# Kernel optimization log

Hardware: AMD Instinct MI355X
Metric: run time of the kernel (lower is better)

## Reference

```python
import jax, jax.numpy as jnp
import numpy as np

DIM = 512
NUM_EXPERTS = 16
HIDDEN = 512
OUT_DIM = DIM // 4  # 128


def setup_inputs() -> dict:
    key = jax.random.key(0)
    k_x, k_w1, k_w2 = jax.random.split(key, 3)
    x = jax.random.normal(k_x, (4, 2048, DIM), dtype=jnp.float32)
    # init_(t): uniform(-1/sqrt(last_dim), 1/sqrt(last_dim))
    s1 = 1.0 / np.sqrt(HIDDEN)
    s2 = 1.0 / np.sqrt(OUT_DIM)
    w1 = jax.random.uniform(k_w1, (NUM_EXPERTS, DIM, HIDDEN), dtype=jnp.float32, minval=-s1, maxval=s1)
    w2 = jax.random.uniform(k_w2, (NUM_EXPERTS, HIDDEN, OUT_DIM), dtype=jnp.float32, minval=-s2, maxval=s2)
    return {"x": x, "w1": w1, "w2": w2}


def reference(x, w1, w2):
    # x: [b, n, d]; w1: [e, d, h]; w2: [e, h, d4]
    hidden = jnp.einsum("bnd,edh->benh", x, w1)          # [b, e, n, h]
    hidden = jax.nn.gelu(hidden, approximate=False)       # exact GELU = torch nn.GELU default
    out = jnp.einsum("benh,ehd->bnde", hidden, w2)        # [b, n, d4, e]
    return out
```

## Files before the change

### kernel.cpp

```cpp
#include <hip/hip_runtime.h>
#include <stdint.h>

typedef short bf16x8 __attribute__((ext_vector_type(8)));
typedef float f32x4 __attribute__((ext_vector_type(4)));

__device__ __forceinline__ void async_cp16(const void* g, short* lds) {
  __builtin_amdgcn_global_load_lds(
      (const __attribute__((address_space(1))) void*)g,
      (__attribute__((address_space(3))) void*)lds, 16, 0, 0);
}

__device__ __forceinline__ float gelu_f(float v) {
  float z = 1.5957691216057308f * (v + 0.044715f * v * v * v);
  return __fdividef(v, 1.0f + __expf(-z));
}

__device__ __forceinline__ short f2bf(float x) {
  uint32_t u = __float_as_uint(x);
  u += 0x7fffu + ((u >> 16) & 1u);
  return (short)(u >> 16);
}

__global__ __launch_bounds__(256)
void prep_all(const float* __restrict__ x, const float* __restrict__ w1,
              const float* __restrict__ w2, short* __restrict__ Xb,
              short* __restrict__ w1t, short* __restrict__ w2t)
{
  __shared__ __align__(16) short T[64][72];
  const int b = blockIdx.x;
  const int t = threadIdx.x;

  if (b < 2048) {
    const int idx = (b * 256 + t) * 8;
    bf16x8 o;
#pragma unroll
    for (int u = 0; u < 8; ++u) o[u] = f2bf(x[idx + u]);
    *(bf16x8*)(Xb + idx) = o;
    return;
  }

  const float* src; short* dst; int e, r0, c0, R, C;
  if (b < 3072) {
    int idx = b - 2048; e = idx >> 6; int rem = idx & 63;
    r0 = (rem >> 3) * 64; c0 = (rem & 7) * 64; R = 512; C = 512;
    src = w1; dst = w1t;
  } else {
    int idx = b - 3072; e = idx >> 4; int rem = idx & 15;
    r0 = (rem >> 1) * 64; c0 = (rem & 1) * 64; R = 512; C = 128;
    src = w2; dst = w2t;
  }
  const float* s = src + (size_t)e * R * C;
  short* d       = dst + (size_t)e * R * C;
  const int i = t >> 3, j8 = t & 7;
#pragma unroll
  for (int p = 0; p < 2; ++p) {
    int ii = i + p * 32;
#pragma unroll
    for (int u = 0; u < 8; ++u)
      T[ii][j8 * 8 + u] = f2bf(s[(size_t)(r0 + ii) * C + c0 + j8 * 8 + u]);
  }
  __syncthreads();
#pragma unroll
  for (int p = 0; p < 2; ++p) {
    int ii = i + p * 32;
    bf16x8 v;
#pragma unroll
    for (int u = 0; u < 8; ++u) v[u] = T[j8 * 8 + u][ii];
    *(bf16x8*)(d + (size_t)(c0 + ii) * R + r0 + j8 * 8) = v;
  }
}

__global__ __launch_bounds__(256, 2)
void moe_kernel(const short* __restrict__ Xb, const short* __restrict__ W1T,
                const short* __restrict__ W2T, float* __restrict__ O, int staged)
{
  __shared__ __align__(16) short SM[33792];
  short* const Xs0 = SM;
  short* const Xs1 = SM + 4096;
  short* const Ws0 = SM + 8192;
  short* const Ws1 = SM + 12288;
  short* const HL  = SM + 16384;

  const int tid = threadIdx.x;
  const int l = tid & 63, w = tid >> 6;
  const int wm = w & 1, wn = w >> 1;
  const int e = blockIdx.x & 15;
  const int tile = blockIdx.x >> 4;

  const int lrow = l >> 2, lq = l & 3;
  int ldso[2];
  const char *xg[2], *w1g[2], *w2g[2];
#pragma unroll
  for (int c = 0; c < 2; ++c) {
    int prow = w * 32 + c * 16 + lrow;
    int qg = lq ^ ((prow >> 1) & 3);
    ldso[c] = (w * 32 + c * 16) * 32;
    xg[c]  = (const char*)Xb  + (size_t)(tile * 128 + prow) * 1024 + qg * 16;
    w1g[c] = (const char*)W1T + (size_t)e * 524288 + (size_t)prow * 1024 + qg * 16;
    w2g[c] = (const char*)W2T + (size_t)e * 131072 + (size_t)prow * 1024 + qg * 16;
  }

  const int lm = l & 15;
  const int slot = (l >> 4) ^ ((lm >> 1) & 3);
  const int aoff = (wm * 64 + lm) * 32 + slot * 8;
  const int boff = (wn * 64 + lm) * 32 + slot * 8;
  const int hro  = (wm * 64 + lm) * 136 + (l >> 4) * 8;
  const int hwo  = (wm * 64 + (l >> 4) * 4) * 136 + wn * 64 + lm;

  f32x4 acc2[4][4];
#pragma unroll
  for (int i = 0; i < 4; ++i)
#pragma unroll
    for (int j = 0; j < 4; ++j) acc2[i][j] = (f32x4){0.f, 0.f, 0.f, 0.f};

#pragma unroll
  for (int c = 0; c < 2; ++c) {
    async_cp16(xg[c],  Xs0 + ldso[c]);
    async_cp16(w1g[c], Ws0 + ldso[c]);
  }

  for (int hc = 0; hc < 4; ++hc) {
    f32x4 acc1[4][4];
#pragma unroll
    for (int i = 0; i < 4; ++i)
#pragma unroll
      for (int j = 0; j < 4; ++j) acc1[i][j] = (f32x4){0.f, 0.f, 0.f, 0.f};

    const size_t w1hc = (size_t)hc * 131072;

#pragma unroll
    for (int kk = 0; kk < 16; ++kk) {
      __syncthreads();
      if (kk < 15) {
        short* xb = ((kk + 1) & 1) ? Xs1 : Xs0;
        short* wb = ((kk + 1) & 1) ? Ws1 : Ws0;
#pragma unroll
        for (int c = 0; c < 2; ++c) {
          async_cp16(xg[c] + (kk + 1) * 64,         xb + ldso[c]);
          async_cp16(w1g[c] + w1hc + (kk + 1) * 64, wb + ldso[c]);
        }
      } else {
#pragma unroll
        for (int c = 0; c < 2; ++c)
          async_cp16(w2g[c] + hc * 256, Ws0 + ldso[c]);
      }
      const short* xb = (kk & 1) ? Xs1 : Xs0;
      const short* wb = (kk & 1) ? Ws1 : Ws0;
      bf16x8 af[4], bfr[4];
#pragma unroll
      for (int t = 0; t < 4; ++t) af[t]  = *(const bf16x8*)(xb + aoff + t * 512);
#pragma unroll
      for (int t = 0; t < 4; ++t) bfr[t] = *(const bf16x8*)(wb + boff + t * 512);
#pragma unroll
      for (int i = 0; i < 4; ++i)
#pragma unroll
        for (int j = 0; j < 4; ++j)
          acc1[i][j] = __builtin_amdgcn_mfma_f32_16x16x32_bf16(af[i], bfr[j], acc1[i][j], 0, 0, 0);
    }

#pragma unroll
    for (int i = 0; i < 4; ++i)
#pragma unroll
      for (int j = 0; j < 4; ++j)
#pragma unroll
        for (int r = 0; r < 4; ++r)
          HL[hwo + i * 2176 + r * 136 + j * 16] = f2bf(gelu_f(acc1[i][j][r]));

#pragma unroll
    for (int s = 0; s < 4; ++s) {
      __syncthreads();
      if (s < 3) {
        short* wb = ((s + 1) & 1) ? Ws1 : Ws0;
#pragma unroll
        for (int c = 0; c < 2; ++c)
          async_cp16(w2g[c] + hc * 256 + (s + 1) * 64, wb + ldso[c]);
      } else if (hc < 3) {
#pragma unroll
        for (int c = 0; c < 2; ++c) {
          async_cp16(xg[c],                              Xs0 + ldso[c]);
          async_cp16(w1g[c] + (size_t)(hc + 1) * 131072, Ws0 + ldso[c]);
        }
      }
      const short* wb = (s & 1) ? Ws1 : Ws0;
      bf16x8 af[4], bfr[4];
#pragma unroll
      for (int t = 0; t < 4; ++t) af[t]  = *(const bf16x8*)(HL + hro + t * 2176 + s * 32);
#pragma unroll
      for (int t = 0; t < 4; ++t) bfr[t] = *(const bf16x8*)(wb + boff + t * 512);
#pragma unroll
      for (int i = 0; i < 4; ++i)
#pragma unroll
        for (int j = 0; j < 4; ++j)
          acc2[i][j] = __builtin_amdgcn_mfma_f32_16x16x32_bf16(af[i], bfr[j], acc2[i][j], 0, 0, 0);
    }
  }

  const int d4 = wn * 64 + lm;
  const int lqr = (l >> 4) * 4;
  if (staged) {
    const size_t base = ((size_t)e * 8192 + tile * 128 + wm * 64 + lqr) * 128 + d4;
#pragma unroll
    for (int i = 0; i < 4; ++i)
#pragma unroll
      for (int r = 0; r < 4; ++r)
#pragma unroll
        for (int j = 0; j < 4; ++j)
          O[base + (size_t)(i * 16 + r) * 128 + j * 16] = acc2[i][j][r];
  } else {
    const size_t rowb = (size_t)tile * 128 + wm * 64 + lqr;
    const size_t base = (rowb * 128 + d4) * 16 + e;
#pragma unroll
    for (int i = 0; i < 4; ++i)
#pragma unroll
      for (int r = 0; r < 4; ++r)
#pragma unroll
        for (int j = 0; j < 4; ++j)
          O[base + (size_t)(i * 16 + r) * 2048 + j * 256] = acc2[i][j][r];
  }
}

__global__ __launch_bounds__(256, 2)
void permute_kernel(const float* __restrict__ OUTs, float* __restrict__ OUT)
{
  __shared__ float T[8 * 16 * 132];
  const int t = threadIdx.x;
  const int r0 = blockIdx.x * 8;
#pragma unroll
  for (int it = 0; it < 16; ++it) {
    int v = it * 256 + t;
    int e = v >> 8, r = (v >> 5) & 7, q = v & 31;
    f32x4 d = *(const f32x4*)(OUTs + ((size_t)e * 8192 + r0 + r) * 128 + q * 4);
    *(f32x4*)(&T[(r * 16 + e) * 132 + q * 4]) = d;
  }
  __syncthreads();
#pragma unroll
  for (int it = 0; it < 16; ++it) {
    int u = it * 256 + t;
    int r = u >> 9;
    int c4 = (u & 511) * 4;
    int d4 = c4 >> 4, e0 = c4 & 15;
    f32x4 o;
#pragma unroll
    for (int i = 0; i < 4; ++i) o[i] = T[(r * 16 + e0 + i) * 132 + d4];
    *(f32x4*)(OUT + (size_t)(r0 + r) * 2048 + c4) = o;
  }
}

extern "C" void kernel_launch(void* const* d_in, const int* in_sizes, int n_in,
                              void* d_out, int out_size, void* d_ws, size_t ws_size,
                              hipStream_t stream)
{
  const float* x  = (const float*)d_in[0];
  const float* w1 = (const float*)d_in[1];
  const float* w2 = (const float*)d_in[2];
  float* out = (float*)d_out;

  short* Xb  = (short*)d_ws;
  short* w1t = Xb + 4194304;
  short* w2t = w1t + 4194304;
  float* OUTs = (float*)((char*)d_ws + 18874368);
  const bool staged = ws_size >= 85983232ULL;

  prep_all<<<dim3(3328), 256, 0, stream>>>(x, w1, w2, Xb, w1t, w2t);
  moe_kernel<<<dim3(1024), 256, 0, stream>>>(Xb, w1t, w2t,
                                             staged ? OUTs : out, staged ? 1 : 0);
  if (staged)
    permute_kernel<<<dim3(1024), 256, 0, stream>>>(OUTs, out);
}
```

Measured before the change: 235.0 us.

## Alias hidden tile onto X buffers for 3 blocks/CU and stage output in bf16

Shrinks shared memory by overlaying the GELU hidden tile on the X double-buffer region and raises the launch bound to 3 blocks per CU. To make the overlay safe, it adds barriers and moves the prefetch of the next hidden chunk's X/W1 tiles to after the second GEMM, which loses the overlap that prefetch used to have. The staged intermediate output is now written as bf16 and widened back to fp32 in the permute kernel, halving that traffic. The bf16 staging adds rounding error to the final output, and a 3-block bound may force register spills given the two 64-float accumulator sets.

```diff
diff --git a/kernel.cpp b/kernel.cpp
--- a/kernel.cpp
+++ b/kernel.cpp
@@ -70,16 +70,16 @@
   }
 }
 
-__global__ __launch_bounds__(256, 2)
+__global__ __launch_bounds__(256, 3)
 void moe_kernel(const short* __restrict__ Xb, const short* __restrict__ W1T,
-                const short* __restrict__ W2T, float* __restrict__ O, int staged)
-{
-  __shared__ __align__(16) short SM[33792];
-  short* const Xs0 = SM;
-  short* const Xs1 = SM + 4096;
-  short* const Ws0 = SM + 8192;
-  short* const Ws1 = SM + 12288;
-  short* const HL  = SM + 16384;
+                const short* __restrict__ W2T, void* __restrict__ O, int staged)
+{
+  __shared__ __align__(16) short SM[25600];
+  short* const Ws0 = SM;
+  short* const Ws1 = SM + 4096;
+  short* const Xs0 = SM + 8192;
+  short* const Xs1 = SM + 12288;
+  short* const HL  = SM + 8192;
 
   const int tid = threadIdx.x;
   const int l = tid & 63, w = tid >> 6;
@@ -158,6 +158,8 @@
           acc1[i][j] = __builtin_amdgcn_mfma_f32_16x16x32_bf16(af[i], bfr[j], acc1[i][j], 0, 0, 0);
     }
 
+    __syncthreads();
+
 #pragma unroll
     for (int i = 0; i < 4; ++i)
 #pragma unroll
@@ -174,12 +176,6 @@
 #pragma unroll
         for (int c = 0; c < 2; ++c)
           async_cp16(w2g[c] + hc * 256 + (s + 1) * 64, wb + ldso[c]);
-      } else if (hc < 3) {
-#pragma unroll
-        for (int c = 0; c < 2; ++c) {
-          async_cp16(xg[c],                              Xs0 + ldso[c]);
-          async_cp16(w1g[c] + (size_t)(hc + 1) * 131072, Ws0 + ldso[c]);
-        }
       }
       const short* wb = (s & 1) ? Ws1 : Ws0;
       bf16x8 af[4], bfr[4];
@@ -193,11 +189,21 @@
         for (int j = 0; j < 4; ++j)
           acc2[i][j] = __builtin_amdgcn_mfma_f32_16x16x32_bf16(af[i], bfr[j], acc2[i][j], 0, 0, 0);
     }
+
+    if (hc < 3) {
+      __syncthreads();
+#pragma unroll
+      for (int c = 0; c < 2; ++c) {
+        async_cp16(xg[c],                              Xs0 + ldso[c]);
+        async_cp16(w1g[c] + (size_t)(hc + 1) * 131072, Ws0 + ldso[c]);
+      }
+    }
   }
 
   const int d4 = wn * 64 + lm;
   const int lqr = (l >> 4) * 4;
   if (staged) {
+    unsigned short* Ob = (unsigned short*)O;
     const size_t base = ((size_t)e * 8192 + tile * 128 + wm * 64 + lqr) * 128 + d4;
 #pragma unroll
     for (int i = 0; i < 4; ++i)
@@ -205,8 +211,9 @@
       for (int r = 0; r < 4; ++r)
 #pragma unroll
         for (int j = 0; j < 4; ++j)
-          O[base + (size_t)(i * 16 + r) * 128 + j * 16] = acc2[i][j][r];
+          Ob[base + (size_t)(i * 16 + r) * 128 + j * 16] = (unsigned short)f2bf(acc2[i][j][r]);
   } else {
+    float* Of = (float*)O;
     const size_t rowb = (size_t)tile * 128 + wm * 64 + lqr;
     const size_t base = (rowb * 128 + d4) * 16 + e;
 #pragma unroll
@@ -215,22 +222,25 @@
       for (int r = 0; r < 4; ++r)
 #pragma unroll
         for (int j = 0; j < 4; ++j)
-          O[base + (size_t)(i * 16 + r) * 2048 + j * 256] = acc2[i][j][r];
+          Of[base + (size_t)(i * 16 + r) * 2048 + j * 256] = acc2[i][j][r];
   }
 }
 
 __global__ __launch_bounds__(256, 2)
-void permute_kernel(const float* __restrict__ OUTs, float* __restrict__ OUT)
+void permute_kernel(const unsigned short* __restrict__ OUTs, float* __restrict__ OUT)
 {
   __shared__ float T[8 * 16 * 132];
   const int t = threadIdx.x;
   const int r0 = blockIdx.x * 8;
 #pragma unroll
-  for (int it = 0; it < 16; ++it) {
+  for (int it = 0; it < 8; ++it) {
     int v = it * 256 + t;
-    int e = v >> 8, r = (v >> 5) & 7, q = v & 31;
-    f32x4 d = *(const f32x4*)(OUTs + ((size_t)e * 8192 + r0 + r) * 128 + q * 4);
-    *(f32x4*)(&T[(r * 16 + e) * 132 + q * 4]) = d;
+    int e = v >> 7, rem = v & 127, r = rem >> 4, q8 = rem & 15;
+    bf16x8 d = *(const bf16x8*)(OUTs + ((size_t)e * 8192 + r0 + r) * 128 + q8 * 8);
+#pragma unroll
+    for (int u = 0; u < 8; ++u)
+      T[(r * 16 + e) * 132 + q8 * 8 + u] =
+          __uint_as_float(((uint32_t)(unsigned short)d[u]) << 16);
   }
   __syncthreads();
 #pragma unroll
@@ -258,12 +268,13 @@
   short* Xb  = (short*)d_ws;
   short* w1t = Xb + 4194304;
   short* w2t = w1t + 4194304;
-  float* OUTs = (float*)((char*)d_ws + 18874368);
-  const bool staged = ws_size >= 85983232ULL;
+  unsigned short* OUTs = (unsigned short*)((char*)d_ws + 18874368);
+  const bool staged = ws_size >= 52428800ULL;
 
   prep_all<<<dim3(3328), 256, 0, stream>>>(x, w1, w2, Xb, w1t, w2t);
   moe_kernel<<<dim3(1024), 256, 0, stream>>>(Xb, w1t, w2t,
-                                             staged ? OUTs : out, staged ? 1 : 0);
+                                             staged ? (void*)OUTs : (void*)out,
+                                             staged ? 1 : 0);
   if (staged)
     permute_kernel<<<dim3(1024), 256, 0, stream>>>(OUTs, out);
 }
```

Result: slower. 326.3 us (+38.8%).
